# Kernel tuning notes

Measured on AMD Instinct MI355X. Metric: run time of the kernel, lower is better.

The kernel has to match this reference:

```python
import jax, jax.numpy as jnp
import numpy as np

D_MODEL = 1024
NUM_HEADS = 16
HEAD_DIM = D_MODEL // NUM_HEADS


def setup_inputs() -> dict:
    key = jax.random.key(0)
    k_x, k_wqkv, k_bqkv, k_wo, k_bo = jax.random.split(key, 5)
    s = 1.0 / np.sqrt(D_MODEL)
    return {
        "x": jax.random.normal(k_x, (4, 2048, D_MODEL), dtype=jnp.float32),
        "W_qkv": jax.random.uniform(k_wqkv, (D_MODEL, 3 * D_MODEL), jnp.float32, -s, s),
        "b_qkv": jax.random.uniform(k_bqkv, (3 * D_MODEL,), jnp.float32, -s, s),
        "W_out": jax.random.uniform(k_wo, (D_MODEL, D_MODEL), jnp.float32, -s, s),
        "b_out": jax.random.uniform(k_bo, (D_MODEL,), jnp.float32, -s, s),
    }


def reference(x, W_qkv, b_qkv, W_out, b_out):
    B, N, C = x.shape
    # fused QKV projection -> [B, N, 3, H, Dh]
    qkv = (x @ W_qkv + b_qkv).reshape(B, N, 3, NUM_HEADS, HEAD_DIM)
    q = jnp.transpose(qkv[:, :, 0], (0, 2, 1, 3))  # [B, H, N, Dh]
    k = jnp.transpose(qkv[:, :, 1], (0, 2, 1, 3))
    v = jnp.transpose(qkv[:, :, 2], (0, 2, 1, 3))
    scale = 1.0 / jnp.sqrt(jnp.asarray(HEAD_DIM, dtype=x.dtype))
    attn = jnp.einsum('bhqd,bhkd->bhqk', q, k) * scale  # [B, H, N, N]
    attn = jax.nn.softmax(attn, axis=-1)
    # dropout is identity in eval mode
    out = jnp.einsum('bhqk,bhkd->bhqd', attn, v)  # [B, H, N, Dh]
    out = jnp.transpose(out, (0, 2, 1, 3)).reshape(B, N, C)
    return out @ W_out + b_out
```

## Files before the change

### kernel.cpp

```cpp
#include <hip/hip_runtime.h>


typedef __bf16 bf16x8 __attribute__((ext_vector_type(8)));
typedef float f32x4 __attribute__((ext_vector_type(4)));
typedef unsigned int u32x4 __attribute__((ext_vector_type(4)));

#define DEV __device__ __forceinline__

DEV unsigned short f2b(float x) {
  unsigned int u = __float_as_uint(x);
  u += 0x7fffu + ((u >> 16) & 1u);
  return (unsigned short)(u >> 16);
}

DEV unsigned int pk_bf16(float a, float b) {
  unsigned int ua = __float_as_uint(a) + 0x8000u;
  unsigned int ub = __float_as_uint(b) + 0x8000u;
  return __builtin_amdgcn_perm(ub, ua, 0x07060302u);
}

#if __has_builtin(__builtin_amdgcn_exp2f)
DEV float exp2_fast(float x) { return __builtin_amdgcn_exp2f(x); }
#else
DEV float exp2_fast(float x) { return exp2f(x); }
#endif

DEV void xpose_pair(unsigned int a, unsigned int b,
                    unsigned int& x, unsigned int& y) {
#if __has_builtin(__builtin_amdgcn_permlane32_swap) && \
    __has_builtin(__builtin_amdgcn_permlane16_swap)
  auto t = __builtin_amdgcn_permlane32_swap(a, b, false, false);
  auto u = __builtin_amdgcn_permlane16_swap(t[0], t[1], false, false);
  x = u[0];
  y = u[1];
#else
  int la = (int)(threadIdx.x & 63);
  unsigned int a32 = (unsigned int)__shfl_xor((int)a, 32, 64);
  unsigned int b32 = (unsigned int)__shfl_xor((int)b, 32, 64);
  unsigned int t0 = (la < 32) ? a : b32;
  unsigned int t1 = (la < 32) ? a32 : b;
  unsigned int t0x = (unsigned int)__shfl_xor((int)t0, 16, 64);
  unsigned int t1x = (unsigned int)__shfl_xor((int)t1, 16, 64);
  bool odd = ((la >> 4) & 1) != 0;
  x = odd ? t1x : t0;
  y = odd ? t1 : t0x;
#endif
}

DEV bf16x8 u4_to_bf(u32x4 v) {
  union { u32x4 u; bf16x8 b; } c;
  c.u = v;
  return c.b;
}

DEV void g2l16(const void* g, void* l) {
  __builtin_amdgcn_global_load_lds(
      (const __attribute__((address_space(1))) unsigned int*)(unsigned long long)g,
      (__attribute__((address_space(3))) unsigned int*)(unsigned int)(unsigned long long)l,
      16, 0, 0);
}

__global__ void cvt_x_kernel(const float* __restrict__ x,
                             unsigned short* __restrict__ xb) {
  int i = blockIdx.x * blockDim.x + threadIdx.x;
  float4 v = ((const float4*)x)[i];
  ushort4 o;
  o.x = f2b(v.x); o.y = f2b(v.y); o.z = f2b(v.z); o.w = f2b(v.w);
  ((ushort4*)xb)[i] = o;
}

__global__ void cvt_wt_kernel(const float* __restrict__ W,
                              unsigned short* __restrict__ Wt,
                              int K, int N) {
  __shared__ float tile[32][33];
  int n0 = blockIdx.x * 32, k0 = blockIdx.y * 32;
  int tx = threadIdx.x, ty = threadIdx.y;
#pragma unroll
  for (int i = 0; i < 32; i += 8)
    tile[ty + i][tx] = W[(size_t)(k0 + ty + i) * N + n0 + tx];
  __syncthreads();
#pragma unroll
  for (int i = 0; i < 32; i += 8)
    Wt[(size_t)(n0 + ty + i) * K + k0 + tx] = f2b(tile[tx][ty + i]);
}

#define QSCALE 0.18033688011112042f

template <int MODE>
__global__ __launch_bounds__(256, 2)
void gemm_bt_kernel(const unsigned short* __restrict__ A,
                    const unsigned short* __restrict__ Bt,
                    const float* __restrict__ bias,
                    unsigned short* __restrict__ qout,
                    unsigned short* __restrict__ kfrout,
                    unsigned short* __restrict__ vfrout,
                    float* __restrict__ fout) {
  constexpr int K = 1024;
  __shared__ unsigned short As[128 * 32];
  __shared__ unsigned short Bs[128 * 32];

  const int tid = threadIdx.x;
  const int lane = tid & 63;
  const int w = tid >> 6;
  const int wm = w & 1, wn = w >> 1;
  const int l15 = lane & 15, quad = lane >> 4;
  const int m0 = blockIdx.y * 128;
  const int n0 = blockIdx.x * 128;

  const unsigned short* Ag = A + (size_t)m0 * K;
  const unsigned short* Bg = Bt + (size_t)n0 * K;

  const int c0 = tid, c1 = tid + 256;
  const size_t ga0 = (size_t)(c0 >> 2) * K + (size_t)(c0 & 3) * 8;
  const size_t ga1 = (size_t)(c1 >> 2) * K + (size_t)(c1 & 3) * 8;
  unsigned short* la0 = &As[c0 * 8];
  unsigned short* la1 = &As[c1 * 8];
  unsigned short* lb0 = &Bs[c0 * 8];
  unsigned short* lb1 = &Bs[c1 * 8];

  f32x4 acc[4][4] = {};

  for (int kt = 0; kt < K; kt += 32) {
    g2l16(Ag + ga0 + kt, la0);
    g2l16(Ag + ga1 + kt, la1);
    g2l16(Bg + ga0 + kt, lb0);
    g2l16(Bg + ga1 + kt, lb1);
    __syncthreads();
    bf16x8 af[4], bfr[4];
#pragma unroll
    for (int i = 0; i < 4; ++i) {
      af[i]  = *(const bf16x8*)&As[(wm * 64 + i * 16 + l15) * 32 + quad * 8];
      bfr[i] = *(const bf16x8*)&Bs[(wn * 64 + i * 16 + l15) * 32 + quad * 8];
    }
#pragma unroll
    for (int mi = 0; mi < 4; ++mi)
#pragma unroll
      for (int ni = 0; ni < 4; ++ni)
        acc[mi][ni] = __builtin_amdgcn_mfma_f32_16x16x32_bf16(
            af[mi], bfr[ni], acc[mi][ni], 0, 0, 0);
    __syncthreads();
  }

  float bv[4];
#pragma unroll
  for (int ni = 0; ni < 4; ++ni)
    bv[ni] = bias[n0 + wn * 64 + ni * 16 + l15];

  if (MODE == 0) {
    const int sel = n0 >> 10;
    const int bbat = m0 >> 11;
    const int ktb = ((m0 & 2047) >> 6) + wm;
    if (sel == 0) {
#pragma unroll
      for (int mi = 0; mi < 4; ++mi) {
        int rb = m0 + wm * 64 + mi * 16 + quad * 4;
#pragma unroll
        for (int ni = 0; ni < 4; ++ni) {
          int c = (n0 & 1023) + wn * 64 + ni * 16 + l15;
#pragma unroll
          for (int r = 0; r < 4; ++r)
            qout[(size_t)(rb + r) * 1024 + c] =
                f2b((acc[mi][ni][r] + bv[ni]) * QSCALE);
        }
      }
    } else if (sel == 1) {
#pragma unroll
      for (int ni = 0; ni < 4; ++ni) {
        int c = (n0 & 1023) + wn * 64 + ni * 16 + l15;
        int h = c >> 6, d = c & 63;
        int kc = d >> 5, dq = (d >> 3) & 3, j = d & 7;
        size_t fb = ((((size_t)(bbat * 16 + h) * 32 + ktb) * 8) + kc) * 512 +
                    (size_t)(dq * 16) * 8 + j;
#pragma unroll
        for (int mi = 0; mi < 4; ++mi) {
          size_t fm = fb + (size_t)mi * 1024;
#pragma unroll
          for (int r = 0; r < 4; ++r)
            kfrout[fm + (quad * 4 + r) * 8] = f2b(acc[mi][ni][r] + bv[ni]);
        }
      }
    } else {
      const int fqb = quad >> 1;
      const int jj0 = (quad & 1) * 4;
#pragma unroll
      for (int ni = 0; ni < 4; ++ni) {
        int c = (n0 & 1023) + wn * 64 + ni * 16 + l15;
        int h = c >> 6, d = c & 63;
        int df = d >> 4, fl15 = d & 15;
#pragma unroll
        for (int mi = 0; mi < 4; ++mi) {
          int kc2 = mi >> 1;
          int fquad = (mi & 1) * 2 + fqb;
          size_t fb = ((((size_t)(bbat * 16 + h) * 32 + ktb) * 8) + df * 2 + kc2) * 512 +
                      (size_t)(fquad * 16 + fl15) * 8 + jj0;
          ushort4 pk;
          pk.x = f2b(acc[mi][ni][0] + bv[ni]);
          pk.y = f2b(acc[mi][ni][1] + bv[ni]);
          pk.z = f2b(acc[mi][ni][2] + bv[ni]);
          pk.w = f2b(acc[mi][ni][3] + bv[ni]);
          *(ushort4*)&vfrout[fb] = pk;
        }
      }
    }
  } else {
#pragma unroll
    for (int mi = 0; mi < 4; ++mi) {
      int rb = m0 + wm * 64 + mi * 16 + quad * 4;
#pragma unroll
      for (int ni = 0; ni < 4; ++ni) {
        int c = n0 + wn * 64 + ni * 16 + l15;
#pragma unroll
        for (int r = 0; r < 4; ++r)
          fout[(size_t)(rb + r) * 1024 + c] = acc[mi][ni][r] + bv[ni];
      }
    }
  }
}

__global__ __launch_bounds__(256, 2)
void attn_kernel(const unsigned short* __restrict__ qg,
                 const unsigned short* __restrict__ kfr,
                 const unsigned short* __restrict__ vfr,
                 unsigned short* __restrict__ oat) {
  const int tid = threadIdx.x;
  const int lane = tid & 63;
  const int w = tid >> 6;
  const int l15 = lane & 15, quad = lane >> 4;

  const int head = blockIdx.x * 8 + (blockIdx.y >> 3);
  const int q0 = (blockIdx.y & 7) * 256;
  const int b = head >> 4, h = head & 15;
  const size_t tokbase = (size_t)b * 2048;

  bf16x8 qf[4][2];
#pragma unroll
  for (int ni = 0; ni < 4; ++ni)
#pragma unroll
    for (int kc = 0; kc < 2; ++kc) {
      int q = q0 + w * 64 + ni * 16 + l15;
      qf[ni][kc] = *(const bf16x8*)(qg + (tokbase + q) * 1024 + h * 64 +
                                    kc * 32 + quad * 8);
    }

  f32x4 oacc[4][4] = {};
  float lsum[4] = {0.f, 0.f, 0.f, 0.f};

  const bf16x8* kp = (const bf16x8*)kfr + (size_t)head * 32 * 512;
  const bf16x8* vp = (const bf16x8*)vfr + (size_t)head * 32 * 512;

  bf16x8 kfA[8], vfA[8];
#pragma unroll
  for (int f = 0; f < 8; ++f) {
    kfA[f] = kp[f * 64 + lane];
    vfA[f] = vp[f * 64 + lane];
  }

#pragma unroll 2
  for (int kt = 0; kt < 32; ++kt) {
    bf16x8 kfB[8], vfB[8];
    if (kt < 31) {
      const bf16x8* kn = kp + (kt + 1) * 512;
      const bf16x8* vn = vp + (kt + 1) * 512;
#pragma unroll
      for (int f = 0; f < 8; ++f) {
        kfB[f] = kn[f * 64 + lane];
        vfB[f] = vn[f * 64 + lane];
      }
    }

#pragma unroll
    for (int nh = 0; nh < 2; ++nh) {
      f32x4 st[4][2];
#pragma unroll
      for (int mi = 0; mi < 4; ++mi)
#pragma unroll
        for (int nj = 0; nj < 2; ++nj)
          st[mi][nj] = (f32x4){0.f, 0.f, 0.f, 0.f};
#pragma unroll
      for (int kc = 0; kc < 2; ++kc)
#pragma unroll
        for (int mi = 0; mi < 4; ++mi)
#pragma unroll
          for (int nj = 0; nj < 2; ++nj)
            st[mi][nj] = __builtin_amdgcn_mfma_f32_16x16x32_bf16(
                kfA[mi * 2 + kc], qf[nh * 2 + nj][kc], st[mi][nj], 0, 0, 0);

      bf16x8 pf2[2][2];
#pragma unroll
      for (int nj = 0; nj < 2; ++nj) {
        int ni = nh * 2 + nj;
        float rs = 0.f;
        unsigned int s0[4], s1[4];
#pragma unroll
        for (int mi = 0; mi < 4; ++mi) {
          float p0 = exp2_fast(st[mi][nj][0]);
          float p1 = exp2_fast(st[mi][nj][1]);
          float p2 = exp2_fast(st[mi][nj][2]);
          float p3 = exp2_fast(st[mi][nj][3]);
          rs += (p0 + p1) + (p2 + p3);
          s0[mi] = pk_bf16(p0, p1);
          s1[mi] = pk_bf16(p2, p3);
        }
        lsum[ni] += rs;
        unsigned int o00, o01, o02, o03, o10, o11, o12, o13;
        xpose_pair(s0[0], s0[1], o00, o02);
        xpose_pair(s1[0], s1[1], o01, o03);
        xpose_pair(s0[2], s0[3], o10, o12);
        xpose_pair(s1[2], s1[3], o11, o13);
        u32x4 t0 = {o00, o01, o02, o03};
        u32x4 t1 = {o10, o11, o12, o13};
        pf2[nj][0] = u4_to_bf(t0);
        pf2[nj][1] = u4_to_bf(t1);
      }

#pragma unroll
      for (int kc = 0; kc < 2; ++kc)
#pragma unroll
        for (int df = 0; df < 4; ++df)
#pragma unroll
          for (int nj = 0; nj < 2; ++nj)
            oacc[df][nh * 2 + nj] = __builtin_amdgcn_mfma_f32_16x16x32_bf16(
                vfA[df * 2 + kc], pf2[nj][kc], oacc[df][nh * 2 + nj], 0, 0, 0);
    }

#pragma unroll
    for (int f = 0; f < 8; ++f) { kfA[f] = kfB[f]; vfA[f] = vfB[f]; }
  }

#pragma unroll
  for (int ni = 0; ni < 4; ++ni) {
    float s = lsum[ni];
    s += __shfl_xor(s, 16, 64);
    s += __shfl_xor(s, 32, 64);
    float inv = __builtin_amdgcn_rcpf(s);
    int q = q0 + w * 64 + ni * 16 + l15;
#pragma unroll
    for (int df = 0; df < 4; ++df) {
      uint2 pw;
      pw.x = pk_bf16(oacc[df][ni][0] * inv, oacc[df][ni][1] * inv);
      pw.y = pk_bf16(oacc[df][ni][2] * inv, oacc[df][ni][3] * inv);
      *(uint2*)&oat[(tokbase + q) * 1024 + h * 64 + df * 16 + quad * 4] = pw;
    }
  }
}

extern "C" void kernel_launch(void* const* d_in, const int* in_sizes, int n_in,
                              void* d_out, int out_size, void* d_ws, size_t ws_size,
                              hipStream_t stream) {
  const float* x    = (const float*)d_in[0];
  const float* Wqkv = (const float*)d_in[1];
  const float* bqkv = (const float*)d_in[2];
  const float* Wout = (const float*)d_in[3];
  const float* bout = (const float*)d_in[4];
  float* out = (float*)d_out;

  char* ws = (char*)d_ws;
  unsigned short* xb  = (unsigned short*)(ws + (size_t)0);
  unsigned short* wqt = (unsigned short*)(ws + ((size_t)16 << 20));
  unsigned short* wot = (unsigned short*)(ws + ((size_t)22 << 20));
  unsigned short* qbf = (unsigned short*)(ws + ((size_t)24 << 20));
  unsigned short* kfr = (unsigned short*)(ws + ((size_t)40 << 20));
  unsigned short* vfr = (unsigned short*)(ws + ((size_t)56 << 20));
  unsigned short* oat = (unsigned short*)(ws + ((size_t)72 << 20));

  cvt_x_kernel<<<8192, 256, 0, stream>>>(x, xb);
  cvt_wt_kernel<<<dim3(96, 32), dim3(32, 8), 0, stream>>>(Wqkv, wqt, 1024, 3072);
  cvt_wt_kernel<<<dim3(32, 32), dim3(32, 8), 0, stream>>>(Wout, wot, 1024, 1024);

  gemm_bt_kernel<0><<<dim3(24, 64), 256, 0, stream>>>(
      xb, wqt, bqkv, qbf, kfr, vfr, nullptr);

  attn_kernel<<<dim3(8, 64), 256, 0, stream>>>(qbf, kfr, vfr, oat);

  gemm_bt_kernel<1><<<dim3(8, 64), 256, 0, stream>>>(
      oat, wot, bout, nullptr, nullptr, nullptr, out);
}
```

Before: 332.0 us.

## Stage K/V tiles through double-buffered LDS and halve attention query tile

The attention kernel now copies each 64-key K/V tile into double-buffered shared memory with async global-to-LDS copies, so all four waves share one load instead of each wave reading the fragments from global memory into registers. The query tile per block drops from 256 to 128 rows and the grid doubles. Register use falls, allowing occupancy hint 4 instead of 2. MFMA blocks are wrapped in s_setprio, and bf16 packing switches from manual rounding to a native cast. The cost is a __syncthreads per key tile and less reuse of each K/V tile per block.

```diff
diff --git a/kernel.cpp b/kernel.cpp
--- a/kernel.cpp
+++ b/kernel.cpp
@@ -13,10 +13,11 @@
   return (unsigned short)(u >> 16);
 }
 
-DEV unsigned int pk_bf16(float a, float b) {
-  unsigned int ua = __float_as_uint(a) + 0x8000u;
-  unsigned int ub = __float_as_uint(b) + 0x8000u;
-  return __builtin_amdgcn_perm(ub, ua, 0x07060302u);
+DEV unsigned int pk2(float a, float b) {
+  union { __bf16 h[2]; unsigned int u; } c;
+  c.h[0] = (__bf16)a;
+  c.h[1] = (__bf16)b;
+  return c.u;
 }
 
 #if __has_builtin(__builtin_amdgcn_exp2f)
@@ -217,128 +218,136 @@
   }
 }
 
-__global__ __launch_bounds__(256, 2)
+__global__ __launch_bounds__(256, 4)
 void attn_kernel(const unsigned short* __restrict__ qg,
                  const unsigned short* __restrict__ kfr,
                  const unsigned short* __restrict__ vfr,
                  unsigned short* __restrict__ oat) {
+  __shared__ unsigned short Ks[2][4096];
+  __shared__ unsigned short Vs[2][4096];
+
   const int tid = threadIdx.x;
   const int lane = tid & 63;
   const int w = tid >> 6;
   const int l15 = lane & 15, quad = lane >> 4;
 
-  const int head = blockIdx.x * 8 + (blockIdx.y >> 3);
-  const int q0 = (blockIdx.y & 7) * 256;
+  const int head = blockIdx.x * 8 + (blockIdx.y >> 4);
+  const int q0 = (blockIdx.y & 15) * 128;
   const int b = head >> 4, h = head & 15;
   const size_t tokbase = (size_t)b * 2048;
 
-  bf16x8 qf[4][2];
-#pragma unroll
-  for (int ni = 0; ni < 4; ++ni)
+  bf16x8 qf[2][2];
+#pragma unroll
+  for (int nj = 0; nj < 2; ++nj)
 #pragma unroll
     for (int kc = 0; kc < 2; ++kc) {
-      int q = q0 + w * 64 + ni * 16 + l15;
-      qf[ni][kc] = *(const bf16x8*)(qg + (tokbase + q) * 1024 + h * 64 +
+      int q = q0 + w * 32 + nj * 16 + l15;
+      qf[nj][kc] = *(const bf16x8*)(qg + (tokbase + q) * 1024 + h * 64 +
                                     kc * 32 + quad * 8);
     }
 
-  f32x4 oacc[4][4] = {};
-  float lsum[4] = {0.f, 0.f, 0.f, 0.f};
-
-  const bf16x8* kp = (const bf16x8*)kfr + (size_t)head * 32 * 512;
-  const bf16x8* vp = (const bf16x8*)vfr + (size_t)head * 32 * 512;
-
-  bf16x8 kfA[8], vfA[8];
-#pragma unroll
-  for (int f = 0; f < 8; ++f) {
-    kfA[f] = kp[f * 64 + lane];
-    vfA[f] = vp[f * 64 + lane];
+  f32x4 oacc[4][2] = {};
+  float lsum[2] = {0.f, 0.f};
+
+  const unsigned short* kpb = kfr + (size_t)head * 32 * 4096;
+  const unsigned short* vpb = vfr + (size_t)head * 32 * 4096;
+
+  auto stage = [&](int buf, int kt2) {
+    const unsigned short* ks = kpb + (size_t)kt2 * 4096;
+    const unsigned short* vs = vpb + (size_t)kt2 * 4096;
+    g2l16(ks + (size_t)tid * 8,         &Ks[buf][tid * 8]);
+    g2l16(ks + (size_t)(tid + 256) * 8, &Ks[buf][(tid + 256) * 8]);
+    g2l16(vs + (size_t)tid * 8,         &Vs[buf][tid * 8]);
+    g2l16(vs + (size_t)(tid + 256) * 8, &Vs[buf][(tid + 256) * 8]);
+  };
+
+  stage(0, 0);
+
+  for (int kt = 0; kt < 32; ++kt) {
+    const int cur = kt & 1;
+    __syncthreads();
+    if (kt < 31) stage(cur ^ 1, kt + 1);
+
+    const unsigned short* Kb = Ks[cur];
+    f32x4 st[2][4];
+#pragma unroll
+    for (int nj = 0; nj < 2; ++nj)
+#pragma unroll
+      for (int mi = 0; mi < 4; ++mi)
+        st[nj][mi] = (f32x4){0.f, 0.f, 0.f, 0.f};
+#pragma unroll
+    for (int kc = 0; kc < 2; ++kc) {
+      bf16x8 kf4[4];
+#pragma unroll
+      for (int mi = 0; mi < 4; ++mi)
+        kf4[mi] = *(const bf16x8*)&Kb[(mi * 2 + kc) * 512 + lane * 8];
+      __builtin_amdgcn_s_setprio(1);
+#pragma unroll
+      for (int mi = 0; mi < 4; ++mi)
+#pragma unroll
+        for (int nj = 0; nj < 2; ++nj)
+          st[nj][mi] = __builtin_amdgcn_mfma_f32_16x16x32_bf16(
+              kf4[mi], qf[nj][kc], st[nj][mi], 0, 0, 0);
+      __builtin_amdgcn_s_setprio(0);
+    }
+
+    bf16x8 pf2[2][2];
+#pragma unroll
+    for (int nj = 0; nj < 2; ++nj) {
+      float rs = 0.f;
+      unsigned int s0[4], s1[4];
+#pragma unroll
+      for (int mi = 0; mi < 4; ++mi) {
+        float p0 = exp2_fast(st[nj][mi][0]);
+        float p1 = exp2_fast(st[nj][mi][1]);
+        float p2 = exp2_fast(st[nj][mi][2]);
+        float p3 = exp2_fast(st[nj][mi][3]);
+        rs += (p0 + p1) + (p2 + p3);
+        s0[mi] = pk2(p0, p1);
+        s1[mi] = pk2(p2, p3);
+      }
+      lsum[nj] += rs;
+      unsigned int o00, o01, o02, o03, o10, o11, o12, o13;
+      xpose_pair(s0[0], s0[1], o00, o02);
+      xpose_pair(s1[0], s1[1], o01, o03);
+      xpose_pair(s0[2], s0[3], o10, o12);
+      xpose_pair(s1[2], s1[3], o11, o13);
+      u32x4 t0 = {o00, o01, o02, o03};
+      u32x4 t1 = {o10, o11, o12, o13};
+      pf2[nj][0] = u4_to_bf(t0);
+      pf2[nj][1] = u4_to_bf(t1);
+    }
+
+    const unsigned short* Vb = Vs[cur];
+#pragma unroll
+    for (int kc = 0; kc < 2; ++kc) {
+      bf16x8 vf4[4];
+#pragma unroll
+      for (int df = 0; df < 4; ++df)
+        vf4[df] = *(const bf16x8*)&Vb[(df * 2 + kc) * 512 + lane * 8];
+      __builtin_amdgcn_s_setprio(1);
+#pragma unroll
+      for (int df = 0; df < 4; ++df)
+#pragma unroll
+        for (int nj = 0; nj < 2; ++nj)
+          oacc[df][nj] = __builtin_amdgcn_mfma_f32_16x16x32_bf16(
+              vf4[df], pf2[nj][kc], oacc[df][nj], 0, 0, 0);
+      __builtin_amdgcn_s_setprio(0);
+    }
   }
 
-#pragma unroll 2
-  for (int kt = 0; kt < 32; ++kt) {
-    bf16x8 kfB[8], vfB[8];
-    if (kt < 31) {
-      const bf16x8* kn = kp + (kt + 1) * 512;
-      const bf16x8* vn = vp + (kt + 1) * 512;
-#pragma unroll
-      for (int f = 0; f < 8; ++f) {
-        kfB[f] = kn[f * 64 + lane];
-        vfB[f] = vn[f * 64 + lane];
-      }
-    }
-
-#pragma unroll
-    for (int nh = 0; nh < 2; ++nh) {
-      f32x4 st[4][2];
-#pragma unroll
-      for (int mi = 0; mi < 4; ++mi)
-#pragma unroll
-        for (int nj = 0; nj < 2; ++nj)
-          st[mi][nj] = (f32x4){0.f, 0.f, 0.f, 0.f};
-#pragma unroll
-      for (int kc = 0; kc < 2; ++kc)
-#pragma unroll
-        for (int mi = 0; mi < 4; ++mi)
-#pragma unroll
-          for (int nj = 0; nj < 2; ++nj)
-            st[mi][nj] = __builtin_amdgcn_mfma_f32_16x16x32_bf16(
-                kfA[mi * 2 + kc], qf[nh * 2 + nj][kc], st[mi][nj], 0, 0, 0);
-
-      bf16x8 pf2[2][2];
-#pragma unroll
-      for (int nj = 0; nj < 2; ++nj) {
-        int ni = nh * 2 + nj;
-        float rs = 0.f;
-        unsigned int s0[4], s1[4];
-#pragma unroll
-        for (int mi = 0; mi < 4; ++mi) {
-          float p0 = exp2_fast(st[mi][nj][0]);
-          float p1 = exp2_fast(st[mi][nj][1]);
-          float p2 = exp2_fast(st[mi][nj][2]);
-          float p3 = exp2_fast(st[mi][nj][3]);
-          rs += (p0 + p1) + (p2 + p3);
-          s0[mi] = pk_bf16(p0, p1);
-          s1[mi] = pk_bf16(p2, p3);
-        }
-        lsum[ni] += rs;
-        unsigned int o00, o01, o02, o03, o10, o11, o12, o13;
-        xpose_pair(s0[0], s0[1], o00, o02);
-        xpose_pair(s1[0], s1[1], o01, o03);
-        xpose_pair(s0[2], s0[3], o10, o12);
-        xpose_pair(s1[2], s1[3], o11, o13);
-        u32x4 t0 = {o00, o01, o02, o03};
-        u32x4 t1 = {o10, o11, o12, o13};
-        pf2[nj][0] = u4_to_bf(t0);
-        pf2[nj][1] = u4_to_bf(t1);
-      }
-
-#pragma unroll
-      for (int kc = 0; kc < 2; ++kc)
-#pragma unroll
-        for (int df = 0; df < 4; ++df)
-#pragma unroll
-          for (int nj = 0; nj < 2; ++nj)
-            oacc[df][nh * 2 + nj] = __builtin_amdgcn_mfma_f32_16x16x32_bf16(
-                vfA[df * 2 + kc], pf2[nj][kc], oacc[df][nh * 2 + nj], 0, 0, 0);
-    }
-
-#pragma unroll
-    for (int f = 0; f < 8; ++f) { kfA[f] = kfB[f]; vfA[f] = vfB[f]; }
-  }
-
-#pragma unroll
-  for (int ni = 0; ni < 4; ++ni) {
-    float s = lsum[ni];
+#pragma unroll
+  for (int nj = 0; nj < 2; ++nj) {
+    float s = lsum[nj];
     s += __shfl_xor(s, 16, 64);
     s += __shfl_xor(s, 32, 64);
     float inv = __builtin_amdgcn_rcpf(s);
-    int q = q0 + w * 64 + ni * 16 + l15;
+    int q = q0 + w * 32 + nj * 16 + l15;
 #pragma unroll
     for (int df = 0; df < 4; ++df) {
       uint2 pw;
-      pw.x = pk_bf16(oacc[df][ni][0] * inv, oacc[df][ni][1] * inv);
-      pw.y = pk_bf16(oacc[df][ni][2] * inv, oacc[df][ni][3] * inv);
+      pw.x = pk2(oacc[df][nj][0] * inv, oacc[df][nj][1] * inv);
+      pw.y = pk2(oacc[df][nj][2] * inv, oacc[df][nj][3] * inv);
       *(uint2*)&oat[(tokbase + q) * 1024 + h * 64 + df * 16 + quad * 4] = pw;
     }
   }
@@ -370,7 +379,7 @@
   gemm_bt_kernel<0><<<dim3(24, 64), 256, 0, stream>>>(
       xb, wqt, bqkv, qbf, kfr, vfr, nullptr);
 
-  attn_kernel<<<dim3(8, 64), 256, 0, stream>>>(qbf, kfr, vfr, oat);
+  attn_kernel<<<dim3(8, 128), 256, 0, stream>>>(qbf, kfr, vfr, oat);
 
   gemm_bt_kernel<1><<<dim3(8, 64), 256, 0, stream>>>(
       oat, wot, bout, nullptr, nullptr, nullptr, out);
```

Measured after the change: 270.2 us. 1.23x faster.
